# Optimization experiments

Hardware: AMD Instinct MI355X
Metric: run time of the kernel (lower is better)

The kernel has to match this reference:

```python
import jax, jax.numpy as jnp
import numpy as np

NEG_INF = -1e30  # stand-in for -inf that is safe under fp16/bf16 softmax


def setup_inputs() -> dict:
    key = jax.random.key(0)
    k1, k2, k3, k4 = jax.random.split(key, 4)
    B, T, C, H = 4, 4096, 1024, 64
    x = jax.random.normal(k1, (B, T, C), dtype=jnp.float32)
    Wq = jax.random.normal(k2, (C, H), dtype=jnp.float32) * (C ** -0.5)
    Wk = jax.random.normal(k3, (C, H), dtype=jnp.float32) * (C ** -0.5)
    Wv = jax.random.normal(k4, (C, H), dtype=jnp.float32) * (C ** -0.5)
    return {"x": x, "Wq": Wq, "Wk": Wk, "Wv": Wv}


def reference(x, Wq, Wk, Wv):
    # x: [B,T,C]; Wq/Wk/Wv: [C,H]
    q = jnp.einsum('btc,ch->bth', x, Wq)
    k = jnp.einsum('btc,ch->bth', x, Wk)
    v = jnp.einsum('btc,ch->bth', x, Wv)
    # NOTE: original module applies NO 1/sqrt(head_size) scaling — faithful here.
    wei = jnp.einsum('bqh,bkh->bqk', q, k)  # [B,T,T]
    T = x.shape[1]
    causal = jnp.tril(jnp.ones((T, T), dtype=bool))
    wei = jnp.where(causal, wei, NEG_INF)
    wei = jax.nn.softmax(wei, axis=-1)
    # dropout: eval-mode identity
    out = jnp.einsum('bqk,bkh->bqh', wei, v)  # [B,T,H]
    return out
```

## Files before the change

kernel.cpp:

```cpp
#include <hip/hip_runtime.h>
#include <hip/hip_fp16.h>


typedef __attribute__((ext_vector_type(8))) short bf16x8;
typedef __attribute__((ext_vector_type(8))) unsigned short u16x8;
typedef __attribute__((ext_vector_type(4))) float f32x4;

__device__ __forceinline__ unsigned short f2bf(float f) {
  unsigned u = __float_as_uint(f);
  u += 0x7fffu + ((u >> 16) & 1u);
  return (unsigned short)(u >> 16);
}
__device__ __forceinline__ float bf2f(unsigned short s) {
  return __uint_as_float(((unsigned)s) << 16);
}
__device__ __forceinline__ unsigned cvt_pk_bf16(float lo, float hi) {
  unsigned r;
  asm("v_cvt_pk_bf16_f32 %0, %1, %2" : "=v"(r) : "v"(lo), "v"(hi));
  return r;
}
__device__ __forceinline__ void gload_lds16(const void* g, void* l) {
  __builtin_amdgcn_global_load_lds(
      (const __attribute__((address_space(1))) unsigned int*)g,
      (__attribute__((address_space(3))) unsigned int*)l, 16, 0, 0);
}
#define KSWZ(row, colb) ((((row) * 128) + (colb)) ^ (((row) & 7) << 4))

__global__ __launch_bounds__(256) void wsplit_kernel(
    const float* __restrict__ Wq, const float* __restrict__ Wk,
    const float* __restrict__ Wv,
    unsigned short* __restrict__ Wth, unsigned short* __restrict__ Wtl) {
  const int fl = blockIdx.x * 256 + threadIdx.x;
  const int lane = fl & 63;
  const int rest = fl >> 6;
  const int nf = rest % 12;
  const int ksq = rest / 12;
  const int n = nf * 16 + (lane & 15);
  const int k0 = ksq * 32 + (lane >> 4) * 8;
  const float* wp = (n < 64) ? Wq : ((n < 128) ? Wk : Wv);
  const int h = n & 63;
  u16x8 hi, lo;
#pragma unroll
  for (int j = 0; j < 8; ++j) {
    float v = wp[(size_t)(k0 + j) * 64 + h];
    unsigned short hh = f2bf(v);
    hi[j] = hh;
    lo[j] = f2bf(v - bf2f(hh));
  }
  const size_t base = (size_t)fl * 8;
  *reinterpret_cast<u16x8*>(&Wth[base]) = hi;
  *reinterpret_cast<u16x8*>(&Wtl[base]) = lo;
}

__device__ __forceinline__ void cvt_store8(unsigned short* dh, unsigned short* dl,
                                           const float4& a, const float4& b) {
  float v[8] = {a.x, a.y, a.z, a.w, b.x, b.y, b.z, b.w};
  uint4 hp, lp;
  unsigned* hpp = reinterpret_cast<unsigned*>(&hp);
  unsigned* lpp = reinterpret_cast<unsigned*>(&lp);
#pragma unroll
  for (int p = 0; p < 4; ++p) {
    const unsigned h = cvt_pk_bf16(v[2 * p], v[2 * p + 1]);
    hpp[p] = h;
    const float h0 = __uint_as_float(h << 16);
    const float h1 = __uint_as_float(h & 0xffff0000u);
    lpp[p] = cvt_pk_bf16(v[2 * p] - h0, v[2 * p + 1] - h1);
  }
  *reinterpret_cast<uint4*>(dh) = hp;
  *reinterpret_cast<uint4*>(dl) = lp;
}

__global__ __launch_bounds__(512) void proj_mfma_kernel(
    const float* __restrict__ x,
    const unsigned short* __restrict__ Wth, const unsigned short* __restrict__ Wtl,
    unsigned short* __restrict__ qh, unsigned short* __restrict__ ql,
    unsigned short* __restrict__ kh, unsigned short* __restrict__ kl,
    unsigned short* __restrict__ vt) {
  __shared__ unsigned short Ah[2][64][72];
  __shared__ unsigned short Al[2][64][72];
  __shared__ float xch[48][256];
  const int tid = threadIdx.x;
  const int w = tid >> 6;
  const int lane = tid & 63;
  const int l16 = lane & 15;
  const int g = lane >> 4;
  const int ks = w >> 2;
  const int wc = w & 3;
  const int row0 = blockIdx.x * 64;
  const int sr = tid >> 3;
  const int sc = (tid & 7) * 8;

  f32x4 acc[4][3];
#pragma unroll
  for (int m = 0; m < 4; ++m)
#pragma unroll
    for (int f = 0; f < 3; ++f) {
      f32x4 z = {0.f, 0.f, 0.f, 0.f};
      acc[m][f] = z;
    }

  const float* xp = &x[(size_t)(row0 + sr) * 1024 + sc];

  float4 x0a = *reinterpret_cast<const float4*>(xp);
  float4 x0b = *reinterpret_cast<const float4*>(xp + 4);
  float4 x1a = *reinterpret_cast<const float4*>(xp + 64);
  float4 x1b = *reinterpret_cast<const float4*>(xp + 68);
  cvt_store8(&Ah[0][sr][sc], &Al[0][sr][sc], x0a, x0b);

#pragma unroll 2
  for (int step = 0; step < 16; ++step) {
    __syncthreads();
    if (step < 14) {
      const float* px = xp + (size_t)(step + 2) * 64;
      if ((step & 1) == 0) {
        x0a = *reinterpret_cast<const float4*>(px);
        x0b = *reinterpret_cast<const float4*>(px + 4);
      } else {
        x1a = *reinterpret_cast<const float4*>(px);
        x1b = *reinterpret_cast<const float4*>(px + 4);
      }
    }
    bf16x8 bh[3], bl[3];
#pragma unroll
    for (int f = 0; f < 3; ++f) {
      const size_t off = ((size_t)(step * 2 + ks) * 12 + (wc * 3 + f)) * 512 + lane * 8;
      bh[f] = *reinterpret_cast<const bf16x8*>(&Wth[off]);
      bl[f] = *reinterpret_cast<const bf16x8*>(&Wtl[off]);
    }
    const int cur = step & 1;
    bf16x8 ah[4], al[4];
#pragma unroll
    for (int m = 0; m < 4; ++m) {
      const int ro = m * 16 + l16;
      const int co = ks * 32 + g * 8;
      ah[m] = *reinterpret_cast<const bf16x8*>(&Ah[cur][ro][co]);
      al[m] = *reinterpret_cast<const bf16x8*>(&Al[cur][ro][co]);
    }
#pragma unroll
    for (int m = 0; m < 4; ++m)
#pragma unroll
      for (int f = 0; f < 3; ++f) {
        acc[m][f] = __builtin_amdgcn_mfma_f32_16x16x32_bf16(ah[m], bh[f], acc[m][f], 0, 0, 0);
        acc[m][f] = __builtin_amdgcn_mfma_f32_16x16x32_bf16(ah[m], bl[f], acc[m][f], 0, 0, 0);
        acc[m][f] = __builtin_amdgcn_mfma_f32_16x16x32_bf16(al[m], bh[f], acc[m][f], 0, 0, 0);
      }
    if (step < 15) {
      if (((step + 1) & 1) == 0)
        cvt_store8(&Ah[cur ^ 1][sr][sc], &Al[cur ^ 1][sr][sc], x0a, x0b);
      else
        cvt_store8(&Ah[cur ^ 1][sr][sc], &Al[cur ^ 1][sr][sc], x1a, x1b);
    }
  }

  __syncthreads();
  if (w >= 4) {
#pragma unroll
    for (int m = 0; m < 4; ++m)
#pragma unroll
      for (int f = 0; f < 3; ++f)
#pragma unroll
        for (int j = 0; j < 4; ++j)
          xch[(m * 3 + f) * 4 + j][(w - 4) * 64 + lane] = acc[m][f][j];
  }
  __syncthreads();
  if (w < 4) {
#pragma unroll
    for (int m = 0; m < 4; ++m)
#pragma unroll
      for (int f = 0; f < 3; ++f)
#pragma unroll
        for (int j = 0; j < 4; ++j)
          acc[m][f][j] += xch[(m * 3 + f) * 4 + j][w * 64 + lane];

    const int b = row0 >> 12;
    const int tbase = row0 & 4095;
#pragma unroll
    for (int m = 0; m < 4; ++m)
#pragma unroll
      for (int f = 0; f < 3; ++f) {
        const int nn = wc * 48 + f * 16;
        if (nn < 64) {
          const int h = nn + l16;
#pragma unroll
          for (int j = 0; j < 4; ++j) {
            const int row = row0 + m * 16 + 4 * g + j;
            const float val = acc[m][f][j];
            const unsigned short hi = f2bf(val);
            qh[(size_t)row * 64 + h] = hi;
            ql[(size_t)row * 64 + h] = f2bf(val - bf2f(hi));
          }
        } else if (nn < 128) {
          const int h = nn - 64 + l16;
#pragma unroll
          for (int j = 0; j < 4; ++j) {
            const int row = row0 + m * 16 + 4 * g + j;
            const float val = acc[m][f][j];
            const unsigned short hi = f2bf(val);
            kh[(size_t)row * 64 + h] = hi;
            kl[(size_t)row * 64 + h] = f2bf(val - bf2f(hi));
          }
        } else {
          const int h = nn - 128 + l16;
          ushort4 pv;
          pv.x = f2bf(acc[m][f][0]);
          pv.y = f2bf(acc[m][f][1]);
          pv.z = f2bf(acc[m][f][2]);
          pv.w = f2bf(acc[m][f][3]);
          const size_t a = ((size_t)b * 64 + h) * 4096 + tbase + m * 16 + 4 * g;
          *reinterpret_cast<ushort4*>(&vt[a]) = pv;
        }
      }
  }
}

template <int PT, int NU_B>
__global__ __launch_bounds__(256) void attn_part_block_kernel(
    const unsigned short* __restrict__ qh, const unsigned short* __restrict__ ql,
    const unsigned short* __restrict__ kh, const unsigned short* __restrict__ kl,
    const unsigned short* __restrict__ vt,
    __half* __restrict__ OP, float* __restrict__ ML) {
  __shared__ __align__(16) unsigned short Khs[2][4096];
  __shared__ __align__(16) unsigned short Kls[2][4096];
  __shared__ __align__(16) unsigned short Vs[2][4096];
  __shared__ __align__(16) unsigned short pbuf[4][2][16][88];
  const int tid = threadIdx.x;
  const int w = tid >> 6;
  const int lane = tid & 63;
  const int l16 = lane & 15;
  const int g = lane >> 4;

  const int bx = blockIdx.x;
  const int xc = bx & 7;
  const int b = xc >> 1;
  const int s = 2 * (bx >> 3) + (xc & 1);
  int k = 0, pref = 0;
  for (;;) {
    const int np = (2 * k + 2 + PT - 1) / PT;
    if (s < pref + np) break;
    pref += np;
    ++k;
  }
  const int j4 = k;
  const int p = s - pref;
  const int ntiles = 2 * j4 + 2;
  const int t0 = p * PT;
  const int t1 = min(ntiles, t0 + PT);
  const int q0 = j4 * 128 + w * 32;
  const size_t rowbase = (size_t)b * 4096;

  const int te0 = w * 64 + lane;
  const int te1 = 256 + w * 64 + lane;
  const int r0_ = te0 >> 3, c80 = (te0 & 7) ^ (r0_ & 7);
  const int r1_ = te1 >> 3, c81 = (te1 & 7) ^ (r1_ & 7);
  const int lo0 = te0 * 16, lo1 = te1 * 16;

  bf16x8 q0hf[2], q0lf[2], q1hf[2], q1lf[2];
#pragma unroll
  for (int ss = 0; ss < 2; ++ss) {
    size_t a0 = (rowbase + q0 + l16) * 64 + ss * 32 + g * 8;
    q0hf[ss] = *reinterpret_cast<const bf16x8*>(&qh[a0]);
    q0lf[ss] = *reinterpret_cast<const bf16x8*>(&ql[a0]);
    size_t a1 = a0 + 16 * 64;
    q1hf[ss] = *reinterpret_cast<const bf16x8*>(&qh[a1]);
    q1lf[ss] = *reinterpret_cast<const bf16x8*>(&ql[a1]);
  }

  f32x4 o0[4], o1[4];
#pragma unroll
  for (int hb = 0; hb < 4; ++hb) {
    f32x4 z = {0.f, 0.f, 0.f, 0.f};
    o0[hb] = z;
    o1[hb] = z;
  }
  float m0 = -1e30f, l0 = 0.f, m1 = -1e30f, l1 = 0.f;

  {
    const int kv0 = t0 * 64;
    gload_lds16(&kh[(rowbase + kv0 + r0_) * 64 + c80 * 8], (char*)Khs[0] + lo0);
    gload_lds16(&kl[(rowbase + kv0 + r0_) * 64 + c80 * 8], (char*)Kls[0] + lo0);
    gload_lds16(&vt[((size_t)b * 64 + r0_) * 4096 + kv0 + c80 * 8], (char*)Vs[0] + lo0);
    gload_lds16(&kh[(rowbase + kv0 + r1_) * 64 + c81 * 8], (char*)Khs[0] + lo1);
    gload_lds16(&kl[(rowbase + kv0 + r1_) * 64 + c81 * 8], (char*)Kls[0] + lo1);
    gload_lds16(&vt[((size_t)b * 64 + r1_) * 4096 + kv0 + c81 * 8], (char*)Vs[0] + lo1);
  }

  int cur = 0;
  for (int t = t0; t < t1; ++t) {
    __syncthreads();
    if (t + 1 < t1) {
      const int kn = (t + 1) * 64;
      gload_lds16(&kh[(rowbase + kn + r0_) * 64 + c80 * 8], (char*)Khs[cur ^ 1] + lo0);
      gload_lds16(&kl[(rowbase + kn + r0_) * 64 + c80 * 8], (char*)Kls[cur ^ 1] + lo0);
      gload_lds16(&vt[((size_t)b * 64 + r0_) * 4096 + kn + c80 * 8], (char*)Vs[cur ^ 1] + lo0);
      gload_lds16(&kh[(rowbase + kn + r1_) * 64 + c81 * 8], (char*)Khs[cur ^ 1] + lo1);
      gload_lds16(&kl[(rowbase + kn + r1_) * 64 + c81 * 8], (char*)Kls[cur ^ 1] + lo1);
      gload_lds16(&vt[((size_t)b * 64 + r1_) * 4096 + kn + c81 * 8], (char*)Vs[cur ^ 1] + lo1);
    }
    const int kv0 = t * 64;

    f32x4 s0[4], s1[4];
#pragma unroll
    for (int kb = 0; kb < 4; ++kb) {
      bf16x8 khf[2], klf[2];
#pragma unroll
      for (int ss = 0; ss < 2; ++ss) {
        const int row = kb * 16 + l16;
        const int colb = ss * 64 + g * 16;
        khf[ss] = *reinterpret_cast<const bf16x8*>((const char*)Khs[cur] + KSWZ(row, colb));
        klf[ss] = *reinterpret_cast<const bf16x8*>((const char*)Kls[cur] + KSWZ(row, colb));
      }
      f32x4 a0 = {0.f, 0.f, 0.f, 0.f};
      f32x4 a1 = {0.f, 0.f, 0.f, 0.f};
#pragma unroll
      for (int ss = 0; ss < 2; ++ss) {
        a0 = __builtin_amdgcn_mfma_f32_16x16x32_bf16(khf[ss], q0hf[ss], a0, 0, 0, 0);
        a0 = __builtin_amdgcn_mfma_f32_16x16x32_bf16(khf[ss], q0lf[ss], a0, 0, 0, 0);
        a0 = __builtin_amdgcn_mfma_f32_16x16x32_bf16(klf[ss], q0hf[ss], a0, 0, 0, 0);
        a1 = __builtin_amdgcn_mfma_f32_16x16x32_bf16(khf[ss], q1hf[ss], a1, 0, 0, 0);
        a1 = __builtin_amdgcn_mfma_f32_16x16x32_bf16(khf[ss], q1lf[ss], a1, 0, 0, 0);
        a1 = __builtin_amdgcn_mfma_f32_16x16x32_bf16(klf[ss], q1hf[ss], a1, 0, 0, 0);
      }
      s0[kb] = a0;
      s1[kb] = a1;
    }
    bf16x8 vf[2][4];
#pragma unroll
    for (int ks = 0; ks < 2; ++ks)
#pragma unroll
      for (int hb = 0; hb < 4; ++hb) {
        const int row = hb * 16 + l16;
        const int colb = ks * 64 + g * 16;
        vf[ks][hb] = *reinterpret_cast<const bf16x8*>((const char*)Vs[cur] + KSWZ(row, colb));
      }
    if (kv0 + 63 > q0) {
#pragma unroll
      for (int kb = 0; kb < 4; ++kb)
#pragma unroll
        for (int jj = 0; jj < 4; ++jj) {
          const int kvg = kv0 + kb * 16 + 4 * g + jj;
          if (kvg > q0 + l16) s0[kb][jj] = -1e30f;
          if (kvg > q0 + 16 + l16) s1[kb][jj] = -1e30f;
        }
    }
    float rm0 = s0[0][0], rm1 = s1[0][0];
#pragma unroll
    for (int kb = 0; kb < 4; ++kb) {
      float c0 = fmaxf(fmaxf(s0[kb][0], s0[kb][1]), fmaxf(s0[kb][2], s0[kb][3]));
      float c1 = fmaxf(fmaxf(s1[kb][0], s1[kb][1]), fmaxf(s1[kb][2], s1[kb][3]));
      rm0 = fmaxf(rm0, c0);
      rm1 = fmaxf(rm1, c1);
    }
    rm0 = fmaxf(rm0, __shfl_xor(rm0, 16));
    rm0 = fmaxf(rm0, __shfl_xor(rm0, 32));
    rm1 = fmaxf(rm1, __shfl_xor(rm1, 16));
    rm1 = fmaxf(rm1, __shfl_xor(rm1, 32));
    const bool r0 = !__all(rm0 - m0 <= 8.f);
    const bool r1 = !__all(rm1 - m1 <= 8.f);
    const float mu0 = r0 ? fmaxf(m0, rm0) : m0;
    const float mu1 = r1 ? fmaxf(m1, rm1) : m1;
    const float al0 = r0 ? __expf(m0 - mu0) : 1.f;
    const float al1 = r1 ? __expf(m1 - mu1) : 1.f;
    float ps0 = 0.f, ps1 = 0.f;
#pragma unroll
    for (int kb = 0; kb < 4; ++kb)
#pragma unroll
      for (int jj = 0; jj < 4; ++jj) {
        const float e0 = __expf(s0[kb][jj] - mu0);
        const float e1 = __expf(s1[kb][jj] - mu1);
        s0[kb][jj] = e0;
        s1[kb][jj] = e1;
        ps0 += e0;
        ps1 += e1;
      }
    ps0 += __shfl_xor(ps0, 16);
    ps0 += __shfl_xor(ps0, 32);
    ps1 += __shfl_xor(ps1, 16);
    ps1 += __shfl_xor(ps1, 32);
    l0 = l0 * al0 + ps0;
    m0 = mu0;
    l1 = l1 * al1 + ps1;
    m1 = mu1;
#pragma unroll
    for (int kb = 0; kb < 4; ++kb) {
      *reinterpret_cast<unsigned*>(&pbuf[w][0][l16][kb * 16 + 4 * g]) =
          cvt_pk_bf16(s0[kb][0], s0[kb][1]);
      *reinterpret_cast<unsigned*>(&pbuf[w][0][l16][kb * 16 + 4 * g + 2]) =
          cvt_pk_bf16(s0[kb][2], s0[kb][3]);
      *reinterpret_cast<unsigned*>(&pbuf[w][1][l16][kb * 16 + 4 * g]) =
          cvt_pk_bf16(s1[kb][0], s1[kb][1]);
      *reinterpret_cast<unsigned*>(&pbuf[w][1][l16][kb * 16 + 4 * g + 2]) =
          cvt_pk_bf16(s1[kb][2], s1[kb][3]);
    }
    if (r0) {
#pragma unroll
      for (int jj = 0; jj < 4; ++jj) {
        const float a0r = __shfl(al0, 4 * g + jj);
#pragma unroll
        for (int hb = 0; hb < 4; ++hb) o0[hb][jj] *= a0r;
      }
    }
    if (r1) {
#pragma unroll
      for (int jj = 0; jj < 4; ++jj) {
        const float a1r = __shfl(al1, 4 * g + jj);
#pragma unroll
        for (int hb = 0; hb < 4; ++hb) o1[hb][jj] *= a1r;
      }
    }
    asm volatile("s_waitcnt lgkmcnt(0)" ::: "memory");
#pragma unroll
    for (int ks = 0; ks < 2; ++ks) {
      bf16x8 pa0 = *reinterpret_cast<const bf16x8*>(&pbuf[w][0][l16][ks * 32 + g * 8]);
      bf16x8 pa1 = *reinterpret_cast<const bf16x8*>(&pbuf[w][1][l16][ks * 32 + g * 8]);
#pragma unroll
      for (int hb = 0; hb < 4; ++hb) {
        o0[hb] = __builtin_amdgcn_mfma_f32_16x16x32_bf16(pa0, vf[ks][hb], o0[hb], 0, 0, 0);
        o1[hb] = __builtin_amdgcn_mfma_f32_16x16x32_bf16(pa1, vf[ks][hb], o1[hb], 0, 0, 0);
      }
    }
    cur ^= 1;
  }

  const size_t u = (size_t)b * NU_B + s;
  __half* op = OP + u * 8192 + (size_t)w * 32 * 64;
#pragma unroll
  for (int jj = 0; jj < 4; ++jj) {
    const int srcr = 4 * g + jj;
    const float l0r = __shfl(l0, srcr);
    const float l1r = __shfl(l1, srcr);
#pragma unroll
    for (int hb = 0; hb < 4; ++hb) {
      op[(4 * g + jj) * 64 + hb * 16 + l16] = __float2half(o0[hb][jj] / l0r);
      op[(16 + 4 * g + jj) * 64 + hb * 16 + l16] = __float2half(o1[hb][jj] / l1r);
    }
  }
  float* ml = ML + u * 256 + w * 64;
  if (lane < 16) {
    ml[lane] = m0;
    ml[32 + lane] = l0;
  } else if (lane < 32) {
    ml[lane] = m1;
    ml[32 + lane] = l1;
  }
}

template <int PT, int NU_B>
__global__ __launch_bounds__(256) void attn_combine_kernel(
    const __half* __restrict__ OP, const float* __restrict__ ML,
    float* __restrict__ out) {
  const int tid = threadIdx.x;
  const int w = tid >> 6;
  const int lane = tid & 63;
  const int rid = blockIdx.x * 4 + w;
  const int b = rid >> 12;
  const int rr = rid & 4095;
  const int j4 = rr >> 7;
  const int local = rr & 127;
  const int nparts = (2 * j4 + 2 + PT - 1) / PT;
  int prefix = 0;
  for (int k = 0; k < j4; ++k) prefix += (2 * k + 2 + PT - 1) / PT;
  const size_t base = (size_t)b * NU_B + prefix;
  const int wv = local >> 5;
  const int tile = (local >> 4) & 1;
  const int rowin = local & 15;
  const int mi = wv * 64 + tile * 16 + rowin;

  float M = -1e30f;
  for (int p = 0; p < nparts; ++p) M = fmaxf(M, ML[(base + p) * 256 + mi]);
  float wsum = 0.f, acc = 0.f;
  for (int p = 0; p < nparts; ++p) {
    const float m = ML[(base + p) * 256 + mi];
    const float l = ML[(base + p) * 256 + 32 + mi];
    const float wg = l * __expf(m - M);
    wsum += wg;
    acc += wg * __half2float(OP[(base + p) * 8192 + (size_t)local * 64 + lane]);
  }
  out[(size_t)rid * 64 + lane] = acc / wsum;
}

extern "C" void kernel_launch(void* const* d_in, const int* in_sizes, int n_in,
                              void* d_out, int out_size, void* d_ws, size_t ws_size,
                              hipStream_t stream) {
  const float* x  = (const float*)d_in[0];
  const float* Wq = (const float*)d_in[1];
  const float* Wk = (const float*)d_in[2];
  const float* Wv = (const float*)d_in[3];
  float* out = (float*)d_out;

  const size_t N = (size_t)4 * 4096 * 64;
  const size_t WN = (size_t)192 * 1024;
  unsigned short* qh = (unsigned short*)d_ws;
  unsigned short* ql = qh + N;
  unsigned short* kh = ql + N;
  unsigned short* kl = kh + N;
  unsigned short* vt = kl + N;
  unsigned short* Wth = vt + N;
  unsigned short* Wtl = Wth + WN;
  __half* OP = (__half*)(Wtl + WN);
  const size_t base_need = (5 * N + 2 * WN) * 2;

  const size_t NU4 = 4 * 272, NU8 = 4 * 144;
  const size_t need4 = base_need + NU4 * 8192 * 2 + NU4 * 256 * 4;
  const size_t need8 = base_need + NU8 * 8192 * 2 + NU8 * 256 * 4;

  wsplit_kernel<<<dim3(96), dim3(256), 0, stream>>>(Wq, Wk, Wv, Wth, Wtl);
  proj_mfma_kernel<<<dim3(256), dim3(512), 0, stream>>>(x, Wth, Wtl, qh, ql, kh, kl, vt);
  if (ws_size >= need4) {
    float* ML = (float*)(OP + NU4 * 8192);
    attn_part_block_kernel<4, 272><<<dim3(NU4), dim3(256), 0, stream>>>(qh, ql, kh, kl, vt, OP, ML);
    attn_combine_kernel<4, 272><<<dim3(4096), dim3(256), 0, stream>>>(OP, ML, out);
  } else {
    float* ML = (float*)(OP + NU8 * 8192);
    attn_part_block_kernel<8, 144><<<dim3(NU8), dim3(256), 0, stream>>>(qh, ql, kh, kl, vt, OP, ML);
    attn_combine_kernel<8, 144><<<dim3(4096), dim3(256), 0, stream>>>(OP, ML, out);
  }
}
```

Baseline: 93.12 us.

## Load x fragments directly into registers in projection, dropping LDS staging

The projection kernel no longer stages x tiles through a double-buffered shared-memory array with per-step barriers. Each wave now loads its own MFMA A-operand rows straight from global memory and splits them into bf16 hi/lo parts in registers. This removes the LDS writes and reads and the __syncthreads in the main loop. In exchange, each x element is loaded and converted redundantly by the four waves sharing a k-slice, there is no prefetch of the next step, and global loads are strided per lane.

```diff
diff --git a/kernel.cpp b/kernel.cpp
--- a/kernel.cpp
+++ b/kernel.cpp
@@ -52,8 +52,8 @@
   *reinterpret_cast<u16x8*>(&Wtl[base]) = lo;
 }
 
-__device__ __forceinline__ void cvt_store8(unsigned short* dh, unsigned short* dl,
-                                           const float4& a, const float4& b) {
+__device__ __forceinline__ void cvt8_reg(const float4& a, const float4& b,
+                                         bf16x8& hi8, bf16x8& lo8) {
   float v[8] = {a.x, a.y, a.z, a.w, b.x, b.y, b.z, b.w};
   uint4 hp, lp;
   unsigned* hpp = reinterpret_cast<unsigned*>(&hp);
@@ -66,8 +66,8 @@
     const float h1 = __uint_as_float(h & 0xffff0000u);
     lpp[p] = cvt_pk_bf16(v[2 * p] - h0, v[2 * p + 1] - h1);
   }
-  *reinterpret_cast<uint4*>(dh) = hp;
-  *reinterpret_cast<uint4*>(dl) = lp;
+  hi8 = *reinterpret_cast<bf16x8*>(&hp);
+  lo8 = *reinterpret_cast<bf16x8*>(&lp);
 }
 
 __global__ __launch_bounds__(512) void proj_mfma_kernel(
@@ -76,8 +76,6 @@
     unsigned short* __restrict__ qh, unsigned short* __restrict__ ql,
     unsigned short* __restrict__ kh, unsigned short* __restrict__ kl,
     unsigned short* __restrict__ vt) {
-  __shared__ unsigned short Ah[2][64][72];
-  __shared__ unsigned short Al[2][64][72];
   __shared__ float xch[48][256];
   const int tid = threadIdx.x;
   const int w = tid >> 6;
@@ -87,8 +85,6 @@
   const int ks = w >> 2;
   const int wc = w & 3;
   const int row0 = blockIdx.x * 64;
-  const int sr = tid >> 3;
-  const int sc = (tid & 7) * 8;
 
   f32x4 acc[4][3];
 #pragma unroll
@@ -99,26 +95,17 @@
       acc[m][f] = z;
     }
 
-  const float* xp = &x[(size_t)(row0 + sr) * 1024 + sc];
-
-  float4 x0a = *reinterpret_cast<const float4*>(xp);
-  float4 x0b = *reinterpret_cast<const float4*>(xp + 4);
-  float4 x1a = *reinterpret_cast<const float4*>(xp + 64);
-  float4 x1b = *reinterpret_cast<const float4*>(xp + 68);
-  cvt_store8(&Ah[0][sr][sc], &Al[0][sr][sc], x0a, x0b);
+  const float* xbase = &x[(size_t)(row0 + l16) * 1024 + ks * 32 + g * 8];
 
 #pragma unroll 2
   for (int step = 0; step < 16; ++step) {
-    __syncthreads();
-    if (step < 14) {
-      const float* px = xp + (size_t)(step + 2) * 64;
-      if ((step & 1) == 0) {
-        x0a = *reinterpret_cast<const float4*>(px);
-        x0b = *reinterpret_cast<const float4*>(px + 4);
-      } else {
-        x1a = *reinterpret_cast<const float4*>(px);
-        x1b = *reinterpret_cast<const float4*>(px + 4);
-      }
+    bf16x8 ah[4], al[4];
+#pragma unroll
+    for (int m = 0; m < 4; ++m) {
+      const float* px = xbase + (size_t)m * 16 * 1024 + (size_t)step * 64;
+      const float4 a = *reinterpret_cast<const float4*>(px);
+      const float4 b = *reinterpret_cast<const float4*>(px + 4);
+      cvt8_reg(a, b, ah[m], al[m]);
     }
     bf16x8 bh[3], bl[3];
 #pragma unroll
@@ -127,15 +114,6 @@
       bh[f] = *reinterpret_cast<const bf16x8*>(&Wth[off]);
       bl[f] = *reinterpret_cast<const bf16x8*>(&Wtl[off]);
     }
-    const int cur = step & 1;
-    bf16x8 ah[4], al[4];
-#pragma unroll
-    for (int m = 0; m < 4; ++m) {
-      const int ro = m * 16 + l16;
-      const int co = ks * 32 + g * 8;
-      ah[m] = *reinterpret_cast<const bf16x8*>(&Ah[cur][ro][co]);
-      al[m] = *reinterpret_cast<const bf16x8*>(&Al[cur][ro][co]);
-    }
 #pragma unroll
     for (int m = 0; m < 4; ++m)
 #pragma unroll
@@ -144,12 +122,6 @@
         acc[m][f] = __builtin_amdgcn_mfma_f32_16x16x32_bf16(ah[m], bl[f], acc[m][f], 0, 0, 0);
         acc[m][f] = __builtin_amdgcn_mfma_f32_16x16x32_bf16(al[m], bh[f], acc[m][f], 0, 0, 0);
       }
-    if (step < 15) {
-      if (((step + 1) & 1) == 0)
-        cvt_store8(&Ah[cur ^ 1][sr][sc], &Al[cur ^ 1][sr][sc], x0a, x0b);
-      else
-        cvt_store8(&Ah[cur ^ 1][sr][sc], &Al[cur ^ 1][sr][sc], x1a, x1b);
-    }
   }
 
   __syncthreads();
```

New measurement: 107.7 us. 1.16x slower.
